# Kernel optimization log

Hardware: AMD Instinct MI355X
Metric: run time of the kernel (lower is better)

The kernel has to match this reference:

```python
import jax, jax.numpy as jnp
import numpy as np

N_GRAPHS = 8192
HIDDEN = 256
N_NODES = 500000


def setup_inputs() -> dict:
    key = jax.random.key(0)
    k1, k2, k3, k4, k5 = jax.random.split(key, 5)
    x = jax.random.normal(k1, (N_NODES, HIDDEN), dtype=jnp.float32)
    batch = jnp.sort(jax.random.randint(k2, (N_NODES,), 0, N_GRAPHS, dtype=jnp.int32))
    # attention MLP params: Linear(H,H) -> tanh -> Linear(H,1)
    s1 = 1.0 / np.sqrt(HIDDEN)
    W1 = jax.random.uniform(k3, (HIDDEN, HIDDEN), minval=-s1, maxval=s1, dtype=jnp.float32)
    b1 = jnp.zeros((HIDDEN,), dtype=jnp.float32)
    W2 = jax.random.uniform(k4, (HIDDEN, 1), minval=-s1, maxval=s1, dtype=jnp.float32)
    b2 = jnp.zeros((1,), dtype=jnp.float32)
    return {"x": x, "batch": batch, "W1": W1, "b1": b1, "W2": W2, "b2": b2}


def reference(x, batch, W1, b1, W2, b2):
    # attention logits: [N, 1]
    h = jnp.tanh(x @ W1 + b1)
    attn_logits = h @ W2 + b2  # [N, 1]
    e = jnp.exp(attn_logits)   # faithful: no max-subtraction in original
    # segment-sum of exp per graph, gathered back per node
    denom = jax.ops.segment_sum(e, batch, num_segments=N_GRAPHS)  # [G, 1]
    attn_weights = e / (denom[batch] + 1e-8)  # [N, 1]
    weighted_x = x * attn_weights             # [N, H]
    graph_embeddings = jax.ops.segment_sum(weighted_x, batch, num_segments=N_GRAPHS)  # [G, H]
    return graph_embeddings
```

## Files before the change

kernel.cpp:

```cpp
#include <hip/hip_runtime.h>

#define N_NODES  500000
#define HIDDEN   256
#define N_GRAPHS 8192
#define NTILES   (N_NODES / 32)
#define NWIN     (N_NODES / 16)
#define PROW     260

typedef float f32x4 __attribute__((ext_vector_type(4)));
typedef short s16x8 __attribute__((ext_vector_type(8)));

__device__ __forceinline__ unsigned short f2bf(float f) {
    unsigned int u = __float_as_uint(f);
    u += 0x7fffu + ((u >> 16) & 1u);
    return (unsigned short)(u >> 16);
}

__global__ void prep_w1_kernel(const float* __restrict__ W1,
                               unsigned short* __restrict__ w1pack) {
    int tid  = blockIdx.x * 256 + threadIdx.x;
    int lane = tid & 63;
    int slot = tid >> 6;
    int wv   = slot >> 5;
    int kt   = (slot >> 2) & 7;
    int ntp  = slot & 3;
    int nt   = wv * 4 + ntp;
    int krow = kt * 32 + ((lane >> 4) & 3) * 8;
    int col  = nt * 16 + (lane & 15);
    unsigned short tmp[8];
#pragma unroll
    for (int j = 0; j < 8; ++j)
        tmp[j] = f2bf(W1[(size_t)(krow + j) * 256 + col]);
    *(uint4*)(w1pack + (size_t)tid * 8) = *(const uint4*)tmp;
}

__global__ void offsets_kernel(const int* __restrict__ batch,
                               int* __restrict__ offsEnd) {
    int g = blockIdx.x * 256 + threadIdx.x;
    if (g >= N_GRAPHS) return;
    int lo = 0, hi = N_NODES;
    while (lo < hi) {
        int mid = (lo + hi) >> 1;
        if (batch[mid] < g + 1) lo = mid + 1; else hi = mid;
    }
    offsEnd[g] = lo;
}

__launch_bounds__(256, 4)
__global__ void fused_kernel(const float* __restrict__ x,
                             const int*   __restrict__ batch,
                             const float* __restrict__ b1,
                             const float* __restrict__ W2,
                             const float* __restrict__ b2,
                             const unsigned short* __restrict__ w1pack,
                             float* __restrict__ preW,
                             float* __restrict__ sufW,
                             float* __restrict__ out) {
    __shared__ unsigned short xbf[32 * 256];
    __shared__ float plds[128];

    const int tid  = threadIdx.x;
    const int wave = tid >> 6;
    const int lane = tid & 63;
    const int cl   = lane & 15;
    const int kgrp = lane >> 4;
    const int base = blockIdx.x * 32;

#pragma unroll
    for (int i = 0; i < 4; ++i) {
        int v   = tid + i * 256;
        int row = v >> 5;
        int cu  = v & 31;
        const float* p = x + (size_t)(base + row) * HIDDEN + cu * 8;
        f32x4 a = *(const f32x4*)p;
        f32x4 c = *(const f32x4*)(p + 4);
        s16x8 w;
        w[0] = (short)f2bf(a[0]); w[1] = (short)f2bf(a[1]);
        w[2] = (short)f2bf(a[2]); w[3] = (short)f2bf(a[3]);
        w[4] = (short)f2bf(c[0]); w[5] = (short)f2bf(c[1]);
        w[6] = (short)f2bf(c[2]); w[7] = (short)f2bf(c[3]);
        *(s16x8*)(xbf + (size_t)(row * 32 + (cu ^ (row & 7))) * 8) = w;
    }

    float b1c[4], w2c[4];
#pragma unroll
    for (int ntp = 0; ntp < 4; ++ntp) {
        int nt = wave * 4 + ntp;
        b1c[ntp] = b1[nt * 16 + cl];
        w2c[ntp] = W2[nt * 16 + cl];
    }
    const float b2v = b2[0];
    __syncthreads();

    float sj[2][4];
#pragma unroll
    for (int rt = 0; rt < 2; ++rt)
#pragma unroll
        for (int j = 0; j < 4; ++j) sj[rt][j] = 0.f;

#pragma unroll
    for (int pass = 0; pass < 4; ++pass) {
        f32x4 acc[2];
        acc[0] = (f32x4){0.f, 0.f, 0.f, 0.f};
        acc[1] = (f32x4){0.f, 0.f, 0.f, 0.f};

#pragma unroll
        for (int kt = 0; kt < 8; ++kt) {
            s16x8 bf = *(const s16x8*)(w1pack +
                ((size_t)(((wave * 8 + kt) * 4 + pass) * 64 + lane) << 3));
#pragma unroll
            for (int rt = 0; rt < 2; ++rt) {
                int row = rt * 16 + cl;
                int cu  = kt * 4 + kgrp;
                s16x8 af = *(const s16x8*)(xbf +
                    (size_t)(row * 32 + (cu ^ (row & 7))) * 8);
                acc[rt] = __builtin_amdgcn_mfma_f32_16x16x32_bf16(
                    af, bf, acc[rt], 0, 0, 0);
            }
        }
        float bb = b1c[pass];
        float ww = w2c[pass];
#pragma unroll
        for (int rt = 0; rt < 2; ++rt)
#pragma unroll
            for (int j = 0; j < 4; ++j) {
                float h = acc[rt][j] + bb;
                h = fminf(fmaxf(h, -15.f), 15.f);
                float e2 = __expf(2.f * h);
                float th = (e2 - 1.f) * __builtin_amdgcn_rcpf(e2 + 1.f);
                sj[rt][j] += th * ww;
            }
    }

#pragma unroll
    for (int m = 1; m < 16; m <<= 1)
#pragma unroll
        for (int rt = 0; rt < 2; ++rt)
#pragma unroll
            for (int j = 0; j < 4; ++j)
                sj[rt][j] += __shfl_xor(sj[rt][j], m, 64);
    if (cl == 0) {
#pragma unroll
        for (int rt = 0; rt < 2; ++rt)
#pragma unroll
            for (int j = 0; j < 4; ++j)
                plds[wave * 32 + rt * 16 + kgrp * 4 + j] = sj[rt][j];
    }
    __syncthreads();

    if (wave < 2) {
        const int ws  = base + wave * 16;
        const int wid = blockIdx.x * 2 + wave;
        int rr = wave * 16 + cl;
        float logit = plds[rr] + plds[32 + rr] + plds[64 + rr] + plds[96 + rr] + b2v;
        float el = __expf(logit);

        int bval = batch[ws + cl];
        const int gfirst = __shfl(bval, 0, 64);
        const int glast  = __shfl(bval, 15, 64);
        const bool eb = (ws > 0) && (batch[ws - 1] == gfirst);
        const bool ef = (ws + 16 < N_NODES) && (batch[ws + 16] == glast);

        f32x4 accv = {0.f, 0.f, 0.f, 0.f};
        float accden = 0.f;
        int gcur = gfirst, sl = 0;
#pragma unroll
        for (int r = 0; r < 16; ++r) {
            int   g  = __shfl(bval, r, 64);
            float er = __shfl(el, r, 64);
            if (g != gcur) {
                bool sb = (sl == 0) && eb;
                if (!sb) {
                    float d = accden + 1e-8f;
                    f32x4 res;
                    res[0] = accv[0] / d; res[1] = accv[1] / d;
                    res[2] = accv[2] / d; res[3] = accv[3] / d;
                    *(f32x4*)(out + (size_t)gcur * HIDDEN + lane * 4) = res;
                } else {
                    *(f32x4*)(preW + (size_t)wid * PROW + lane * 4) = accv;
                    if (lane == 0) preW[(size_t)wid * PROW + 256] = accden;
                }
                accv = (f32x4){0.f, 0.f, 0.f, 0.f};
                accden = 0.f;
                gcur = g; sl = r;
            }
            f32x4 xv = *(const f32x4*)(x + (size_t)(ws + r) * HIDDEN + lane * 4);
            accv += er * xv;
            accden += er;
        }
        {
            bool sb = (sl == 0) && eb;
            if (!sb && !ef) {
                float d = accden + 1e-8f;
                f32x4 res;
                res[0] = accv[0] / d; res[1] = accv[1] / d;
                res[2] = accv[2] / d; res[3] = accv[3] / d;
                *(f32x4*)(out + (size_t)gcur * HIDDEN + lane * 4) = res;
            } else if (!sb && sl > 0) {
                *(f32x4*)(sufW + (size_t)wid * PROW + lane * 4) = accv;
                if (lane == 0) sufW[(size_t)wid * PROW + 256] = accden;
            } else {
                *(f32x4*)(preW + (size_t)wid * PROW + lane * 4) = accv;
                if (lane == 0) preW[(size_t)wid * PROW + 256] = accden;
            }
        }
    }
}

__launch_bounds__(256)
__global__ void combine_kernel(const float* __restrict__ preW,
                               const float* __restrict__ sufW,
                               const int* __restrict__ offsEnd,
                               float* __restrict__ out) {
    const int g    = blockIdx.x * 4 + (threadIdx.x >> 6);
    const int lane = threadIdx.x & 63;
    if (g >= N_GRAPHS) return;
    const int s = (g == 0) ? 0 : offsEnd[g - 1];
    const int e = offsEnd[g];
    if (e == s) {
        *(f32x4*)(out + (size_t)g * HIDDEN + lane * 4) = (f32x4){0.f, 0.f, 0.f, 0.f};
        return;
    }
    const int w0 = s >> 4, w1 = (e - 1) >> 4;
    if (w0 == w1) return;

    const float* row = (s > (w0 << 4)) ? sufW + (size_t)w0 * PROW
                                       : preW + (size_t)w0 * PROW;
    f32x4 acc = *(const f32x4*)(row + lane * 4);
    float den = row[256];
    for (int w = w0 + 1; w <= w1; ++w) {
        const float* pr = preW + (size_t)w * PROW;
        acc += *(const f32x4*)(pr + lane * 4);
        den += pr[256];
    }
    float d = den + 1e-8f;
    f32x4 res;
    res[0] = acc[0] / d; res[1] = acc[1] / d;
    res[2] = acc[2] / d; res[3] = acc[3] / d;
    *(f32x4*)(out + (size_t)g * HIDDEN + lane * 4) = res;
}

extern "C" void kernel_launch(void* const* d_in, const int* in_sizes, int n_in,
                              void* d_out, int out_size, void* d_ws, size_t ws_size,
                              hipStream_t stream) {
    const float* x     = (const float*)d_in[0];
    const int*   batch = (const int*)d_in[1];
    const float* W1    = (const float*)d_in[2];
    const float* b1    = (const float*)d_in[3];
    const float* W2    = (const float*)d_in[4];
    const float* b2    = (const float*)d_in[5];
    float* out = (float*)d_out;

    unsigned short* w1pack = (unsigned short*)d_ws;
    int*   offsEnd = (int*)((char*)d_ws + 131072);
    float* preW    = (float*)((char*)d_ws + 163840);
    float* sufW    = (float*)((char*)d_ws + 163840 + (size_t)NWIN * PROW * 4);

    prep_w1_kernel<<<32, 256, 0, stream>>>(W1, w1pack);
    offsets_kernel<<<32, 256, 0, stream>>>(batch, offsEnd);

    fused_kernel<<<NTILES, 256, 0, stream>>>(x, batch, b1, W2, b2, w1pack,
                                             preW, sufW, out);
    combine_kernel<<<(N_GRAPHS + 3) / 4, 256, 0, stream>>>(preW, sufW, offsEnd, out);
}
```

Baseline: 221.5 us.

## Process 64 nodes per block so each W1 fragment load feeds four row tiles

Doubles the node tile per block from 32 to 64 rows, so each wave issues four MFMAs per W1 fragment load instead of two. All four waves now run the segment-reduction epilogue instead of only two, and the batch index loads are issued before the first barrier to hide their latency. Bounds checks handle the ragged last tile. This cuts global W1 traffic per node and idle waves, at the cost of twice the LDS per block and more accumulator registers, which may lower occupancy under the launch bounds.

```diff
diff --git a/kernel.cpp b/kernel.cpp
--- a/kernel.cpp
+++ b/kernel.cpp
@@ -3,7 +3,7 @@
 #define N_NODES  500000
 #define HIDDEN   256
 #define N_GRAPHS 8192
-#define NTILES   (N_NODES / 32)
+#define NTILES   ((N_NODES + 63) / 64)
 #define NWIN     (N_NODES / 16)
 #define PROW     260
 
@@ -56,24 +56,28 @@
                              float* __restrict__ preW,
                              float* __restrict__ sufW,
                              float* __restrict__ out) {
-    __shared__ unsigned short xbf[32 * 256];
-    __shared__ float plds[128];
+    __shared__ unsigned short xbf[64 * 256];
+    __shared__ float plds[256];
 
     const int tid  = threadIdx.x;
     const int wave = tid >> 6;
     const int lane = tid & 63;
     const int cl   = lane & 15;
     const int kgrp = lane >> 4;
-    const int base = blockIdx.x * 32;
-
-#pragma unroll
-    for (int i = 0; i < 4; ++i) {
+    const int base = blockIdx.x * 64;
+
+#pragma unroll
+    for (int i = 0; i < 8; ++i) {
         int v   = tid + i * 256;
         int row = v >> 5;
         int cu  = v & 31;
-        const float* p = x + (size_t)(base + row) * HIDDEN + cu * 8;
-        f32x4 a = *(const f32x4*)p;
-        f32x4 c = *(const f32x4*)(p + 4);
+        f32x4 a = {0.f, 0.f, 0.f, 0.f}, c = {0.f, 0.f, 0.f, 0.f};
+        int node = base + row;
+        if (node < N_NODES) {
+            const float* p = x + (size_t)node * HIDDEN + cu * 8;
+            a = *(const f32x4*)p;
+            c = *(const f32x4*)(p + 4);
+        }
         s16x8 w;
         w[0] = (short)f2bf(a[0]); w[1] = (short)f2bf(a[1]);
         w[2] = (short)f2bf(a[2]); w[3] = (short)f2bf(a[3]);
@@ -82,6 +86,15 @@
         *(s16x8*)(xbf + (size_t)(row * 32 + (cu ^ (row & 7))) * 8) = w;
     }
 
+    const int ws = base + wave * 16;
+    const bool wvalid = (ws < N_NODES);
+    int bval = 0, bprev = -1, bnext = -1;
+    if (wvalid) {
+        bval  = batch[ws + cl];
+        bprev = (ws > 0) ? batch[ws - 1] : -1;
+        bnext = (ws + 16 < N_NODES) ? batch[ws + 16] : -1;
+    }
+
     float b1c[4], w2c[4];
 #pragma unroll
     for (int ntp = 0; ntp < 4; ++ntp) {
@@ -92,24 +105,25 @@
     const float b2v = b2[0];
     __syncthreads();
 
-    float sj[2][4];
-#pragma unroll
-    for (int rt = 0; rt < 2; ++rt)
+    float sj[4][4];
+#pragma unroll
+    for (int rt = 0; rt < 4; ++rt)
 #pragma unroll
         for (int j = 0; j < 4; ++j) sj[rt][j] = 0.f;
 
 #pragma unroll
     for (int pass = 0; pass < 4; ++pass) {
-        f32x4 acc[2];
-        acc[0] = (f32x4){0.f, 0.f, 0.f, 0.f};
-        acc[1] = (f32x4){0.f, 0.f, 0.f, 0.f};
+        f32x4 acc[4];
+#pragma unroll
+        for (int rt = 0; rt < 4; ++rt)
+            acc[rt] = (f32x4){0.f, 0.f, 0.f, 0.f};
 
 #pragma unroll
         for (int kt = 0; kt < 8; ++kt) {
             s16x8 bf = *(const s16x8*)(w1pack +
                 ((size_t)(((wave * 8 + kt) * 4 + pass) * 64 + lane) << 3));
 #pragma unroll
-            for (int rt = 0; rt < 2; ++rt) {
+            for (int rt = 0; rt < 4; ++rt) {
                 int row = rt * 16 + cl;
                 int cu  = kt * 4 + kgrp;
                 s16x8 af = *(const s16x8*)(xbf +
@@ -121,7 +135,7 @@
         float bb = b1c[pass];
         float ww = w2c[pass];
 #pragma unroll
-        for (int rt = 0; rt < 2; ++rt)
+        for (int rt = 0; rt < 4; ++rt)
 #pragma unroll
             for (int j = 0; j < 4; ++j) {
                 float h = acc[rt][j] + bb;
@@ -135,31 +149,29 @@
 #pragma unroll
     for (int m = 1; m < 16; m <<= 1)
 #pragma unroll
-        for (int rt = 0; rt < 2; ++rt)
+        for (int rt = 0; rt < 4; ++rt)
 #pragma unroll
             for (int j = 0; j < 4; ++j)
                 sj[rt][j] += __shfl_xor(sj[rt][j], m, 64);
     if (cl == 0) {
 #pragma unroll
-        for (int rt = 0; rt < 2; ++rt)
+        for (int rt = 0; rt < 4; ++rt)
 #pragma unroll
             for (int j = 0; j < 4; ++j)
-                plds[wave * 32 + rt * 16 + kgrp * 4 + j] = sj[rt][j];
+                plds[wave * 64 + rt * 16 + kgrp * 4 + j] = sj[rt][j];
     }
     __syncthreads();
 
-    if (wave < 2) {
-        const int ws  = base + wave * 16;
-        const int wid = blockIdx.x * 2 + wave;
+    if (wvalid) {
+        const int wid = blockIdx.x * 4 + wave;
         int rr = wave * 16 + cl;
-        float logit = plds[rr] + plds[32 + rr] + plds[64 + rr] + plds[96 + rr] + b2v;
+        float logit = plds[rr] + plds[64 + rr] + plds[128 + rr] + plds[192 + rr] + b2v;
         float el = __expf(logit);
 
-        int bval = batch[ws + cl];
         const int gfirst = __shfl(bval, 0, 64);
         const int glast  = __shfl(bval, 15, 64);
-        const bool eb = (ws > 0) && (batch[ws - 1] == gfirst);
-        const bool ef = (ws + 16 < N_NODES) && (batch[ws + 16] == glast);
+        const bool eb = (bprev == gfirst);
+        const bool ef = (bnext == glast);
 
         f32x4 accv = {0.f, 0.f, 0.f, 0.f};
         float accden = 0.f;
```

Result: slower. 279.0 us (+25.9%).
